# Kernel tuning notes

Hardware: AMD Instinct MI355X
Metric: run time of the kernel (lower is better)

The kernel has to match this reference:

```python
import jax, jax.numpy as jnp
import numpy as np

K = 3
P = 14
INV_SQRT2 = 0.7071067811865476  # db1 (Haar) filter coefficient
EPS = 1e-4


def _pool(x):
    # adaptive_avg_pool2d to (P, P); H, W divisible by P -> uniform mean pooling
    N, C, H, W = x.shape
    return x.reshape(N, C, P, H // P, P, W // P).mean(axis=(3, 5))


def setup_inputs() -> dict:
    key = jax.random.key(0)
    ks = jax.random.split(key, 8)
    N, C, H, W = 64, 3, 224, 224
    D, Cin = 540, 30  # D_clip=D_hidden=540, n_bands*3 = 30
    return {
        "frames": jax.random.normal(ks[0], (N, C, H, W), jnp.float32),
        "t_clip": jax.random.normal(ks[1], (N, D, P, P), jnp.float32),
        "w1": jax.random.normal(ks[2], (D, Cin), jnp.float32) * 0.05,
        "b1": jnp.zeros((D,), jnp.float32),
        "w2": jax.random.normal(ks[3], (D, D), jnp.float32) * 0.05,
        "b2": jnp.zeros((D,), jnp.float32),
        "wg": jax.random.normal(ks[4], (D, 2 * D, 3, 3), jnp.float32) * 0.05,
        "bg": jnp.zeros((D,), jnp.float32),
    }


def reference(frames, t_clip, w1, b1, w2, b2, wg, bg):
    # Batched Haar SWT2 (a trous, periodic), levels 1..K, fully vectorized over
    # (N, C) -- replaces the per-frame/per-channel pywt.swt2 CPU loop.
    a = frames
    bands = []  # per level: HL (cH), LH (cV), HH (cD), each (N, C, H, W)
    for j in range(K):
        d = 2 ** j  # filter dilation at level j+1
        lx = (a + jnp.roll(a, -d, axis=-1)) * INV_SQRT2
        hx = (a - jnp.roll(a, -d, axis=-1)) * INV_SQRT2
        cA = (lx + jnp.roll(lx, -d, axis=-2)) * INV_SQRT2
        cH = (lx - jnp.roll(lx, -d, axis=-2)) * INV_SQRT2
        cV = (hx + jnp.roll(hx, -d, axis=-2)) * INV_SQRT2
        cD = (hx - jnp.roll(hx, -d, axis=-2)) * INV_SQRT2
        bands += [cH, cV, cD]
        a = cA
    # per-(frame, channel) 99th-percentile normalization + pool to (P, P)
    pooled = []
    for b in bands:
        s = jnp.quantile(jnp.abs(b), 0.99, axis=(-2, -1), keepdims=True)
        pooled.append(_pool(b / (s + EPS)))
    # LL band (level K approximation): mean-center then quantile-scale
    mu = a.mean(axis=(-2, -1), keepdims=True)
    s = jnp.quantile(jnp.abs(a - mu), 0.99, axis=(-2, -1), keepdims=True)
    pooled.append(_pool((a - mu) / (s + EPS)))
    e_pix = jnp.concatenate(pooled, axis=1)  # (N, 30, P, P)

    # 1x1 conv -> relu -> 1x1 conv -> tanh
    h = jax.nn.relu(jnp.einsum("ncpq,dc->ndpq", e_pix, w1) + b1[None, :, None, None])
    m = jnp.tanh(jnp.einsum("ncpq,dc->ndpq", h, w2) + b2[None, :, None, None])

    # gated fusion with CLIP patch tokens
    gi = jnp.concatenate([t_clip, m], axis=1)  # (N, 2*D, P, P)
    g = jax.lax.conv_general_dilated(
        gi, wg, (1, 1), "SAME", dimension_numbers=("NCHW", "OIHW", "NCHW")
    ) + bg[None, :, None, None]
    gamma = jax.nn.sigmoid(g)
    return t_clip + gamma * m
```

## Files before the change

kernel.cpp:

```cpp
#include <hip/hip_runtime.h>

typedef unsigned short u16;
typedef unsigned int u32;
typedef __bf16 bf16x8 __attribute__((ext_vector_type(8)));
typedef float f32x4 __attribute__((ext_vector_type(4)));

constexpr int NB = 64, CH3 = 3;
constexpr int PLANES = NB * CH3;
constexpr int PPIX = 224 * 224;
constexpr int PP = 196;
constexpr int NPX = NB * PP;
constexpr int K2 = 576;
constexpr int CIPAD = 1088;
constexpr int KCONV = 9 * CIPAD;
constexpr int BINS = 256;
constexpr int BIN0 = 896;
constexpr int RANK1 = 49674;
constexpr int RANK2 = 49675;

constexpr size_t OFF_HIST = 0;
constexpr size_t SZ_HIST  = (size_t)10 * PLANES * BINS * 4;
constexpr size_t OFF_SUMS = OFF_HIST + SZ_HIST;
constexpr size_t OFF_INVS = OFF_SUMS + 768;
constexpr size_t OFF_BSUM = OFF_INVS + 7680;
constexpr size_t SZ_BSUM  = (size_t)10 * PLANES * PP * 4;
constexpr size_t OFF_EPIX = OFF_BSUM + SZ_BSUM;
constexpr size_t OFF_HBF  = OFF_EPIX + (size_t)NPX * 32 * 4;
constexpr size_t OFF_GIT  = OFF_HBF + (size_t)NPX * K2 * 2;
constexpr size_t SZ_GIT   = (size_t)NB * 256 * CIPAD * 2;
constexpr size_t OFF_WGB  = OFF_GIT + SZ_GIT;
constexpr size_t OFF_W2B  = OFF_WGB + (size_t)640 * KCONV * 2;
constexpr size_t OFF_MARR = OFF_W2B + (size_t)640 * K2 * 2;

__device__ __forceinline__ u16 f2bf(float x) {
  union { float f; u32 u; } c; c.f = x;
  u32 r = c.u + 0x7FFFu + ((c.u >> 16) & 1u);
  return (u16)(r >> 16);
}

__device__ __forceinline__ float wred64(float v) {
  v += __shfl_down(v, 32, 64); v += __shfl_down(v, 16, 64);
  v += __shfl_down(v, 8, 64);  v += __shfl_down(v, 4, 64);
  v += __shfl_down(v, 2, 64);  v += __shfl_down(v, 1, 64);
  return v;
}

__device__ __forceinline__ float gred16(float v) {
  v += __shfl_down(v, 8, 16); v += __shfl_down(v, 4, 16);
  v += __shfl_down(v, 2, 16); v += __shfl_down(v, 1, 16);
  return v;
}

__device__ __forceinline__ int hbin(float v) {
  int b = (int)(__float_as_uint(fabsf(v)) >> 20) - BIN0;
  return min(max(b, 0), BINS - 1);
}

__device__ __forceinline__ void cp16(const void* g, void* l) {
  __builtin_amdgcn_global_load_lds((const __attribute__((address_space(1))) u32*)g,
                                   (__attribute__((address_space(3))) u32*)l, 16, 0, 0);
}

#define BAR_MEM() asm volatile("s_barrier" ::: "memory")

constexpr int RSTRIDE = 10 * 128 + 8;
__global__ __launch_bounds__(256) void swt_fused_kernel(const float* __restrict__ frames,
    float* __restrict__ sums, int* __restrict__ hist, float* __restrict__ bsum)
{
  __shared__ float a1[22 * 224];
  __shared__ float a2[20 * 224];
  __shared__ u32 lh[8 * RSTRIDE];
  __shared__ float csum[14 * 10];
  __shared__ float wsum[4];
  const int t = threadIdx.x;
  const int rb = blockIdx.x, plane = blockIdx.y;
  const float* Pp = frames + (size_t)plane * PPIX;

  for (int i = t; i < 8 * RSTRIDE; i += 256) lh[i] = 0;
  __syncthreads();

  u32* lhr = &lh[(t & 7) * RSTRIDE];
  const int cell0 = (t >> 4) * 10;
  float ps = 0.f;

  if (t < 224) {
    int c2 = t + 1; if (c2 >= 224) c2 -= 224;
    float sH = 0.f, sV = 0.f, sD = 0.f;
    int gr0 = rb * 16; if (gr0 >= 224) gr0 -= 224;
    float q00 = Pp[gr0 * 224 + t], q01 = Pp[gr0 * 224 + c2];
    for (int r = 0; r < 22; ++r) {
      int gr1 = rb * 16 + r + 1; if (gr1 >= 224) gr1 -= 224;
      float p10 = Pp[gr1 * 224 + t], p11 = Pp[gr1 * 224 + c2];
      float sa = q00 + q01, sb = p10 + p11, da = q00 - q01, db = p10 - p11;
      a1[r * 224 + t] = (sa + sb) * 0.5f;
      if (r < 16) {
        float cH = (sa - sb) * 0.5f, cV = (da + db) * 0.5f, cD = (da - db) * 0.5f;
        int bH = hbin(cH), bV = hbin(cV), bD = hbin(cD);
        atomicAdd(&lhr[0 * 128 + (bH >> 1)], 1u << ((bH & 1) * 16));
        atomicAdd(&lhr[1 * 128 + (bV >> 1)], 1u << ((bV & 1) * 16));
        atomicAdd(&lhr[2 * 128 + (bD >> 1)], 1u << ((bD & 1) * 16));
        sH += cH; sV += cV; sD += cD;
        ps += q00;
      }
      q00 = p10; q01 = p11;
    }
    sH = gred16(sH); sV = gred16(sV); sD = gred16(sD);
    if ((t & 15) == 0) { csum[cell0 + 0] = sH; csum[cell0 + 1] = sV; csum[cell0 + 2] = sD; }
  }
  ps = wred64(ps);
  if ((t & 63) == 0) wsum[t >> 6] = ps;
  __syncthreads();
  if (t == 0) atomicAdd(&sums[plane], wsum[0] + wsum[1] + wsum[2] + wsum[3]);

  if (t < 224) {
    int c2 = t + 2; if (c2 >= 224) c2 -= 224;
    float sH = 0.f, sV = 0.f, sD = 0.f;
    for (int r = 0; r < 20; ++r) {
      float p00 = a1[r * 224 + t], p01 = a1[r * 224 + c2];
      float p10 = a1[(r + 2) * 224 + t], p11 = a1[(r + 2) * 224 + c2];
      float sa = p00 + p01, sb = p10 + p11, da = p00 - p01, db = p10 - p11;
      a2[r * 224 + t] = (sa + sb) * 0.5f;
      if (r < 16) {
        float cH = (sa - sb) * 0.5f, cV = (da + db) * 0.5f, cD = (da - db) * 0.5f;
        int bH = hbin(cH), bV = hbin(cV), bD = hbin(cD);
        atomicAdd(&lhr[3 * 128 + (bH >> 1)], 1u << ((bH & 1) * 16));
        atomicAdd(&lhr[4 * 128 + (bV >> 1)], 1u << ((bV & 1) * 16));
        atomicAdd(&lhr[5 * 128 + (bD >> 1)], 1u << ((bD & 1) * 16));
        sH += cH; sV += cV; sD += cD;
      }
    }
    sH = gred16(sH); sV = gred16(sV); sD = gred16(sD);
    if ((t & 15) == 0) { csum[cell0 + 3] = sH; csum[cell0 + 4] = sV; csum[cell0 + 5] = sD; }
  }
  __syncthreads();

  if (t < 224) {
    int c2 = t + 4; if (c2 >= 224) c2 -= 224;
    float sH = 0.f, sV = 0.f, sD = 0.f, sA = 0.f;
    for (int r = 0; r < 16; ++r) {
      float p00 = a2[r * 224 + t], p01 = a2[r * 224 + c2];
      float p10 = a2[(r + 4) * 224 + t], p11 = a2[(r + 4) * 224 + c2];
      float sa = p00 + p01, sb = p10 + p11, da = p00 - p01, db = p10 - p11;
      float cA = (sa + sb) * 0.5f;
      float cH = (sa - sb) * 0.5f, cV = (da + db) * 0.5f, cD = (da - db) * 0.5f;
      int bH = hbin(cH), bV = hbin(cV), bD = hbin(cD), bA = hbin(cA);
      atomicAdd(&lhr[6 * 128 + (bH >> 1)], 1u << ((bH & 1) * 16));
      atomicAdd(&lhr[7 * 128 + (bV >> 1)], 1u << ((bV & 1) * 16));
      atomicAdd(&lhr[8 * 128 + (bD >> 1)], 1u << ((bD & 1) * 16));
      atomicAdd(&lhr[9 * 128 + (bA >> 1)], 1u << ((bA & 1) * 16));
      sH += cH; sV += cV; sD += cD; sA += cA;
    }
    sH = gred16(sH); sV = gred16(sV); sD = gred16(sD); sA = gred16(sA);
    if ((t & 15) == 0) {
      csum[cell0 + 6] = sH; csum[cell0 + 7] = sV; csum[cell0 + 8] = sD; csum[cell0 + 9] = sA;
    }
  }
  __syncthreads();

  for (int i = t; i < 10 * 256; i += 256) {
    int bg = i >> 8, b = i & 255;
    u32 acc = 0;
#pragma unroll
    for (int rp = 0; rp < 8; ++rp)
      acc += (lh[rp * RSTRIDE + bg * 128 + (b >> 1)] >> ((b & 1) * 16)) & 0xFFFFu;
    if (acc) atomicAdd(&hist[((size_t)bg * PLANES + plane) * BINS + b], (int)acc);
  }
  if (t < 140) {
    int cell = t / 10, bg = t - cell * 10;
    bsum[((size_t)bg * PLANES + plane) * PP + rb * 14 + cell] = csum[cell * 10 + bg];
  }
}

__global__ __launch_bounds__(256) void quant_kernel(const int* __restrict__ hist,
    float* __restrict__ invs)
{
  const int g = blockIdx.x;
  __shared__ int cum[BINS];
  __shared__ float vv[2];
  const int t = threadIdx.x;
  const int c = hist[(size_t)g * BINS + t];
  cum[t] = c;
  __syncthreads();
  for (int off = 1; off < BINS; off <<= 1) {
    int y = (t >= off) ? cum[t - off] : 0;
    __syncthreads();
    cum[t] += y;
    __syncthreads();
  }
  int inc = cum[t], prev = inc - c;
#pragma unroll
  for (int k = 0; k < 2; ++k) {
    int rank = k ? RANK2 : RANK1;
    if (prev < rank && rank <= inc) {
      float lo = __uint_as_float((u32)(t + BIN0) << 20);
      float hi = __uint_as_float((u32)(t + BIN0 + 1) << 20);
      float fr = ((float)(rank - prev) - 0.5f) / (float)c;
      fr = fminf(fmaxf(fr, 0.f), 1.f);
      vv[k] = lo + (hi - lo) * fr;
    }
  }
  __syncthreads();
  if (t == 0) {
    float s = 0.75f * vv[0] + 0.25f * vv[1];
    invs[g] = 1.f / (s + 1e-4f);
  }
}

__global__ __launch_bounds__(256) void epix_kernel(const float* __restrict__ bsum,
    const float* __restrict__ sums, const float* __restrict__ invs, float* __restrict__ epix)
{
  int tid = blockIdx.x * 256 + threadIdx.x;
  int ch = tid & 31, px = tid >> 5;
  int n = px / PP, q = px - n * PP;
  float val = 0.f;
  if (ch < 27) {
    int bg = ch / 3, c = ch - bg * 3;
    int plane = n * 3 + c;
    val = bsum[((size_t)bg * PLANES + plane) * PP + q] * (1.f / 256.f) * invs[bg * PLANES + plane];
  } else if (ch < 30) {
    int c = ch - 27, plane = n * 3 + c;
    float mu = sums[plane] * (8.f / 50176.f);
    val = (bsum[((size_t)9 * PLANES + plane) * PP + q] * (1.f / 256.f) - mu) * invs[9 * PLANES + plane];
  }
  epix[tid] = val;
}

__global__ __launch_bounds__(256) void zero_halo_kernel(u16* __restrict__ git)
{
  constexpr int CPB = 136;
  constexpr int CPN = 60 * CPB + 196;
  int tid = blockIdx.x * 256 + threadIdx.x;
  if (tid >= NB * CPN) return;
  int n = tid / CPN, rem = tid - n * CPN;
  int y, x, c;
  if (rem < 60 * CPB) {
    int bi = rem / CPB; c = rem - bi * CPB;
    if (bi < 16) { y = 0; x = bi; }
    else if (bi < 32) { y = 15; x = bi - 16; }
    else { int i = bi - 32; y = 1 + (i >> 1); x = (i & 1) * 15; }
  } else {
    int q = rem - 60 * CPB;
    y = 1 + q / 14; x = 1 + q % 14; c = 135;
  }
  f32x4 z = (f32x4){0.f, 0.f, 0.f, 0.f};
  *reinterpret_cast<f32x4*>(&git[((size_t)(n * 256 + y * 16 + x)) * CIPAD + c * 8]) = z;
}

__global__ __launch_bounds__(256) void pack_wg_kernel(const float* __restrict__ wg,
    u16* __restrict__ wgb)
{
  __shared__ float w[9720];
  const int oc = blockIdx.x;
  const int t = threadIdx.x;
  if (oc < 540) {
    for (int i = t; i < 9720; i += 256) w[i] = wg[(size_t)oc * 9720 + i];
  }
  __syncthreads();
  for (int j = t; j < KCONV; j += 256) {
    int kc = j >> 6, i = j & 63;
    int cib = kc / 9, tap = kc - cib * 9;
    int ci = cib * 64 + i;
    float v = (oc < 540 && ci < 1080) ? w[ci * 9 + tap] : 0.f;
    wgb[(size_t)oc * KCONV + j] = f2bf(v);
  }
}

__global__ __launch_bounds__(256) void pack_w2_kernel(const float* __restrict__ w2,
    u16* __restrict__ w2b)
{
  int tid = blockIdx.x * 256 + threadIdx.x;
  int oc = tid / K2, cc = tid - oc * K2;
  float v = (oc < 540 && cc < 540) ? w2[oc * 540 + cc] : 0.f;
  w2b[tid] = f2bf(v);
}

__global__ __launch_bounds__(256) void fill_git_kernel(const float* __restrict__ tclip,
    u16* __restrict__ git)
{
  __shared__ float tile[64][65];
  const int n = blockIdx.z, ct = blockIdx.y, qt = blockIdx.x;
  const int t = threadIdx.x, tr = t >> 6, tc = t & 63;
#pragma unroll 4
  for (int i = 0; i < 16; ++i) {
    int ci = ct * 64 + i * 4 + tr, q = qt * 64 + tc;
    float v = (ci < 540 && q < 196) ? tclip[((size_t)n * 540 + ci) * 196 + q] : 0.f;
    tile[i * 4 + tr][tc] = v;
  }
  __syncthreads();
#pragma unroll 4
  for (int i = 0; i < 16; ++i) {
    int q = qt * 64 + i * 4 + tr, ci = ct * 64 + tc;
    if (q < 196 && ci < 540) {
      int y = q / 14, x = q - y * 14;
      git[(((size_t)n * 16 + 1 + y) * 16 + 1 + x) * CIPAD + ci] = f2bf(tile[tc][i * 4 + tr]);
    }
  }
}

__global__ __launch_bounds__(256) void gemm1_kernel(const float* __restrict__ epix,
    const float* __restrict__ w1, const float* __restrict__ b1, u16* __restrict__ hbf)
{
  __shared__ float es[64][33];
  __shared__ float w1s[128][33];
  const int t = threadIdx.x;
  const int px0 = blockIdx.x * 64, oc0 = blockIdx.y * 128;
  for (int i = t; i < 64 * 32; i += 256) { int r = i >> 5, cc = i & 31; es[r][cc] = epix[(size_t)(px0 + r) * 32 + cc]; }
  for (int i = t; i < 128 * 32; i += 256) {
    int r = i >> 5, cc = i & 31; int oc = oc0 + r;
    w1s[r][cc] = (oc < 540 && cc < 30) ? w1[oc * 30 + cc] : 0.f;
  }
  __syncthreads();
  const int ocl = t & 31, pxl = (t >> 5) * 8;
  float acc[4][8];
#pragma unroll
  for (int i = 0; i < 4; ++i)
#pragma unroll
    for (int j = 0; j < 8; ++j) acc[i][j] = 0.f;
  for (int k = 0; k < 30; ++k) {
    float wv[4], ev[8];
#pragma unroll
    for (int i = 0; i < 4; ++i) wv[i] = w1s[ocl + 32 * i][k];
#pragma unroll
    for (int j = 0; j < 8; ++j) ev[j] = es[pxl + j][k];
#pragma unroll
    for (int i = 0; i < 4; ++i)
#pragma unroll
      for (int j = 0; j < 8; ++j) acc[i][j] += wv[i] * ev[j];
  }
#pragma unroll
  for (int i = 0; i < 4; ++i) {
    int oc = oc0 + ocl + 32 * i;
    if (oc >= 576) continue;
    float bv = (oc < 540) ? b1[oc] : 0.f;
#pragma unroll
    for (int j = 0; j < 8; ++j) {
      int px = px0 + pxl + j;
      float v = (oc < 540) ? fmaxf(acc[i][j] + bv, 0.f) : 0.f;
      hbf[(size_t)px * K2 + oc] = f2bf(v);
    }
  }
}

template <int MODE>
__global__ __launch_bounds__(256) void mfma_gemm_kernel(
    const u16* __restrict__ A, const u16* __restrict__ Bm,
    const float* __restrict__ bias,
    float* __restrict__ marr, u16* __restrict__ git,
    const float* __restrict__ tclip, float* __restrict__ outp)
{
  constexpr int KCPB = (MODE == 1) ? 153 : 9;
  constexpr int BSTRIDE = (MODE == 1) ? KCONV : K2;
  __shared__ u16 smem[32768];
  const int t = threadIdx.x;
  const int lane = t & 63, wave = t >> 6;
  const int wm = wave & 1, wn = wave >> 1;

  int px0, oc0;
  if constexpr (MODE == 1) {
    int orig = blockIdx.x;
    int xcd = orig & 7, off = orig >> 3;
    constexpr int q = 61, r = 2;
    int wg = (xcd < r ? xcd * (q + 1) : r * (q + 1) + (xcd - r) * q) + off;
    int bx = wg / 5, by = wg - bx * 5;
    px0 = bx * 128; oc0 = by * 128;
  } else {
    px0 = blockIdx.x * 128; oc0 = blockIdx.y * 128;
  }

  const u16* aSrc[4];
  const u16* bSrc[4];
  int dstOff[4];
#pragma unroll
  for (int r = 0; r < 4; ++r) {
    int slot = r * 256 + t;
    int row = slot >> 3;
    int gs = ((slot ^ row) & 7) << 3;
    if constexpr (MODE == 0) {
      aSrc[r] = A + (size_t)(px0 + row) * K2 + gs;
    } else {
      int px = px0 + row;
      int n = px / 196, q2 = px - n * 196;
      int y = q2 / 14, x = q2 - y * 14;
      aSrc[r] = A + (size_t)((n * 16 + y) * 16 + x) * CIPAD + gs;
    }
    bSrc[r] = Bm + (size_t)(oc0 + row) * BSTRIDE + gs;
    dstOff[r] = (r * 256 + wave * 64) * 8;
  }

  auto stage = [&](int kcg, int buf) {
    int boff = kcg * 64;
    int aoff;
    if constexpr (MODE == 1) {
      int cib = kcg / 9, tap = kcg - cib * 9;
      int ky = tap / 3, kx = tap - ky * 3;
      aoff = (ky * 16 + kx) * CIPAD + cib * 64;
    } else aoff = boff;
    u16* As = smem + buf * 16384;
    u16* Bs = As + 8192;
#pragma unroll
    for (int r = 0; r < 4; ++r) cp16(aSrc[r] + aoff, As + dstOff[r]);
#pragma unroll
    for (int r = 0; r < 4; ++r) cp16(bSrc[r] + boff, Bs + dstOff[r]);
  };

  const int tx = lane & 15, quad = lane >> 4, l7 = lane & 7;
  int rowA[4], rowB[4];
#pragma unroll
  for (int i = 0; i < 4; ++i) {
    rowA[i] = (wm * 64 + i * 16 + tx) * 64;
    rowB[i] = (wn * 64 + i * 16 + tx) * 64;
  }

  f32x4 acc[4][4];
#pragma unroll
  for (int i = 0; i < 4; ++i)
#pragma unroll
    for (int j = 0; j < 4; ++j) acc[i][j] = (f32x4){0.f, 0.f, 0.f, 0.f};

  stage(0, 0);
  stage(1, 1);
  int cur = 0;
  for (int kc = 0; kc < KCPB; ++kc) {
    if (kc + 1 < KCPB) { asm volatile("s_waitcnt vmcnt(8)" ::: "memory"); }
    else               { asm volatile("s_waitcnt vmcnt(0)" ::: "memory"); }
    BAR_MEM();
    const u16* As = smem + cur * 16384;
    const u16* Bs = As + 8192;
#pragma unroll
    for (int ks = 0; ks < 2; ++ks) {
      int goff = (((ks * 4 + quad) ^ l7) << 3);
      bf16x8 af[4], bfr[4];
#pragma unroll
      for (int i = 0; i < 4; ++i) af[i] = *reinterpret_cast<const bf16x8*>(As + rowA[i] + goff);
#pragma unroll
      for (int i = 0; i < 4; ++i) bfr[i] = *reinterpret_cast<const bf16x8*>(Bs + rowB[i] + goff);
      __builtin_amdgcn_s_setprio(1);
#pragma unroll
      for (int i = 0; i < 4; ++i)
#pragma unroll
        for (int j = 0; j < 4; ++j)
          acc[i][j] = __builtin_amdgcn_mfma_f32_16x16x32_bf16(af[i], bfr[j], acc[i][j], 0, 0, 0);
      __builtin_amdgcn_s_setprio(0);
    }
    BAR_MEM();
    if (kc + 2 < KCPB) stage(kc + 2, cur);
    cur ^= 1;
  }

#pragma unroll
  for (int j = 0; j < 4; ++j) {
    int oc = oc0 + wn * 64 + j * 16 + tx;
    if (oc >= 540) continue;
    float bv = bias[oc];
#pragma unroll
    for (int i = 0; i < 4; ++i) {
      f32x4 v = acc[i][j];
      int px = px0 + wm * 64 + i * 16 + quad * 4;
      int n = px / 196, q2 = px - n * 196;
      size_t idx = ((size_t)(n * 540 + oc)) * 196 + q2;
      if constexpr (MODE == 0) {
#pragma unroll
        for (int r = 0; r < 4; ++r) {
          float val = tanhf(v[r] + bv);
          marr[idx + r] = val;
          int qq = q2 + r;
          int y = qq / 14, x = qq - y * 14;
          git[((n * 16 + 1 + y) * 16 + 1 + x) * CIPAD + 540 + oc] = f2bf(val);
        }
      } else {
        f32x4 mv = *reinterpret_cast<const f32x4*>(marr + idx);
        f32x4 tv = *reinterpret_cast<const f32x4*>(tclip + idx);
        f32x4 res;
#pragma unroll
        for (int r = 0; r < 4; ++r) {
          float g = v[r] + bv;
          res[r] = tv[r] + mv[r] / (1.f + expf(-g));
        }
        *reinterpret_cast<f32x4*>(outp + idx) = res;
      }
    }
  }
}

extern "C" void kernel_launch(void* const* d_in, const int* in_sizes, int n_in,
                              void* d_out, int out_size, void* d_ws, size_t ws_size,
                              hipStream_t stream)
{
  const float* frames = (const float*)d_in[0];
  const float* t_clip = (const float*)d_in[1];
  const float* w1 = (const float*)d_in[2];
  const float* b1 = (const float*)d_in[3];
  const float* w2 = (const float*)d_in[4];
  const float* b2 = (const float*)d_in[5];
  const float* wg = (const float*)d_in[6];
  const float* bg = (const float*)d_in[7];
  float* out = (float*)d_out;
  char* ws = (char*)d_ws;

  int* HIST = (int*)(ws + OFF_HIST);
  float* SUMS = (float*)(ws + OFF_SUMS);
  float* INVS = (float*)(ws + OFF_INVS);
  float* BSUM = (float*)(ws + OFF_BSUM);
  float* EPIX = (float*)(ws + OFF_EPIX);
  u16* HBF = (u16*)(ws + OFF_HBF);
  u16* GIT = (u16*)(ws + OFF_GIT);
  u16* WGB = (u16*)(ws + OFF_WGB);
  u16* W2B = (u16*)(ws + OFF_W2B);
  float* MARR = (float*)(ws + OFF_MARR);

  hipMemsetAsync(ws + OFF_HIST, 0, SZ_HIST + 768, stream);

  zero_halo_kernel<<<(NB * (60 * 136 + 196) + 255) / 256, 256, 0, stream>>>(GIT);
  pack_wg_kernel<<<640, 256, 0, stream>>>(wg, WGB);
  pack_w2_kernel<<<1440, 256, 0, stream>>>(w2, W2B);
  fill_git_kernel<<<dim3(4, 9, 64), 256, 0, stream>>>(t_clip, GIT);

  swt_fused_kernel<<<dim3(14, PLANES), 256, 0, stream>>>(frames, SUMS, HIST, BSUM);
  quant_kernel<<<1920, 256, 0, stream>>>(HIST, INVS);
  epix_kernel<<<1568, 256, 0, stream>>>(BSUM, SUMS, INVS, EPIX);

  gemm1_kernel<<<dim3(196, 5), 256, 0, stream>>>(EPIX, w1, b1, HBF);
  mfma_gemm_kernel<0><<<dim3(98, 5), 256, 0, stream>>>(HBF, W2B, b2, MARR, GIT, nullptr, nullptr);
  mfma_gemm_kernel<1><<<490, 256, 0, stream>>>(GIT, WGB, bg, MARR, nullptr, t_clip, out);
}
```

Measured before the change: 484.5 us.

## Load GEMM A fragments directly from global, merge pack kernels, fuse epix into gemm1

The MFMA GEMM kernels no longer stage the A operand (activations / im2col'd input) through LDS. Each lane reads its bf16x8 fragments straight from global memory, while B stays double-buffered in LDS, which halves shared memory and the async-copy count. The three weight-pack and halo-zero kernels become one launch, and the epix normalization is computed inside gemm1's tile load, which removes a kernel and an intermediate buffer. The risk is that uncached, uncoalesced per-lane global A loads in the big conv GEMM expose latency and cost bandwidth that LDS staging used to hide.

New measurement: 671.8 us. 38.6% more time.

```diff
diff --git a/kernel.cpp b/kernel.cpp
--- a/kernel.cpp
+++ b/kernel.cpp
@@ -206,72 +206,50 @@
   }
 }
 
-__global__ __launch_bounds__(256) void epix_kernel(const float* __restrict__ bsum,
-    const float* __restrict__ sums, const float* __restrict__ invs, float* __restrict__ epix)
-{
-  int tid = blockIdx.x * 256 + threadIdx.x;
-  int ch = tid & 31, px = tid >> 5;
-  int n = px / PP, q = px - n * PP;
-  float val = 0.f;
-  if (ch < 27) {
-    int bg = ch / 3, c = ch - bg * 3;
-    int plane = n * 3 + c;
-    val = bsum[((size_t)bg * PLANES + plane) * PP + q] * (1.f / 256.f) * invs[bg * PLANES + plane];
-  } else if (ch < 30) {
-    int c = ch - 27, plane = n * 3 + c;
-    float mu = sums[plane] * (8.f / 50176.f);
-    val = (bsum[((size_t)9 * PLANES + plane) * PP + q] * (1.f / 256.f) - mu) * invs[9 * PLANES + plane];
-  }
-  epix[tid] = val;
-}
-
-__global__ __launch_bounds__(256) void zero_halo_kernel(u16* __restrict__ git)
-{
-  constexpr int CPB = 136;
-  constexpr int CPN = 60 * CPB + 196;
-  int tid = blockIdx.x * 256 + threadIdx.x;
-  if (tid >= NB * CPN) return;
-  int n = tid / CPN, rem = tid - n * CPN;
-  int y, x, c;
-  if (rem < 60 * CPB) {
-    int bi = rem / CPB; c = rem - bi * CPB;
-    if (bi < 16) { y = 0; x = bi; }
-    else if (bi < 32) { y = 15; x = bi - 16; }
-    else { int i = bi - 32; y = 1 + (i >> 1); x = (i & 1) * 15; }
+__global__ __launch_bounds__(256) void pack_all_kernel(const float* __restrict__ wg,
+    const float* __restrict__ w2, u16* __restrict__ wgb, u16* __restrict__ w2b,
+    u16* __restrict__ git)
+{
+  __shared__ float w[9720];
+  const int bid = blockIdx.x;
+  const int t = threadIdx.x;
+  if (bid < 640) {
+    const int oc = bid;
+    if (oc < 540) {
+      for (int i = t; i < 9720; i += 256) w[i] = wg[(size_t)oc * 9720 + i];
+    }
+    __syncthreads();
+    for (int j = t; j < KCONV; j += 256) {
+      int kc = j >> 6, i = j & 63;
+      int cib = kc / 9, tap = kc - cib * 9;
+      int ci = cib * 64 + i;
+      float v = (oc < 540 && ci < 1080) ? w[ci * 9 + tap] : 0.f;
+      wgb[(size_t)oc * KCONV + j] = f2bf(v);
+    }
+  } else if (bid < 2080) {
+    int tid = (bid - 640) * 256 + t;
+    int oc = tid / K2, cc = tid - oc * K2;
+    float v = (oc < 540 && cc < 540) ? w2[oc * 540 + cc] : 0.f;
+    w2b[tid] = f2bf(v);
   } else {
-    int q = rem - 60 * CPB;
-    y = 1 + q / 14; x = 1 + q % 14; c = 135;
-  }
-  f32x4 z = (f32x4){0.f, 0.f, 0.f, 0.f};
-  *reinterpret_cast<f32x4*>(&git[((size_t)(n * 256 + y * 16 + x)) * CIPAD + c * 8]) = z;
-}
-
-__global__ __launch_bounds__(256) void pack_wg_kernel(const float* __restrict__ wg,
-    u16* __restrict__ wgb)
-{
-  __shared__ float w[9720];
-  const int oc = blockIdx.x;
-  const int t = threadIdx.x;
-  if (oc < 540) {
-    for (int i = t; i < 9720; i += 256) w[i] = wg[(size_t)oc * 9720 + i];
-  }
-  __syncthreads();
-  for (int j = t; j < KCONV; j += 256) {
-    int kc = j >> 6, i = j & 63;
-    int cib = kc / 9, tap = kc - cib * 9;
-    int ci = cib * 64 + i;
-    float v = (oc < 540 && ci < 1080) ? w[ci * 9 + tap] : 0.f;
-    wgb[(size_t)oc * KCONV + j] = f2bf(v);
-  }
-}
-
-__global__ __launch_bounds__(256) void pack_w2_kernel(const float* __restrict__ w2,
-    u16* __restrict__ w2b)
-{
-  int tid = blockIdx.x * 256 + threadIdx.x;
-  int oc = tid / K2, cc = tid - oc * K2;
-  float v = (oc < 540 && cc < 540) ? w2[oc * 540 + cc] : 0.f;
-  w2b[tid] = f2bf(v);
+    constexpr int CPB = 136;
+    constexpr int CPN = 60 * CPB + 196;
+    int tid = (bid - 2080) * 256 + t;
+    if (tid >= NB * CPN) return;
+    int n = tid / CPN, rem = tid - n * CPN;
+    int y, x, c;
+    if (rem < 60 * CPB) {
+      int bi = rem / CPB; c = rem - bi * CPB;
+      if (bi < 16) { y = 0; x = bi; }
+      else if (bi < 32) { y = 15; x = bi - 16; }
+      else { int i = bi - 32; y = 1 + (i >> 1); x = (i & 1) * 15; }
+    } else {
+      int q = rem - 60 * CPB;
+      y = 1 + q / 14; x = 1 + q % 14; c = 135;
+    }
+    f32x4 z = (f32x4){0.f, 0.f, 0.f, 0.f};
+    *reinterpret_cast<f32x4*>(&git[((size_t)(n * 256 + y * 16 + x)) * CIPAD + c * 8]) = z;
+  }
 }
 
 __global__ __launch_bounds__(256) void fill_git_kernel(const float* __restrict__ tclip,
@@ -297,14 +275,29 @@
   }
 }
 
-__global__ __launch_bounds__(256) void gemm1_kernel(const float* __restrict__ epix,
+__global__ __launch_bounds__(256) void gemm1_kernel(const float* __restrict__ bsum,
+    const float* __restrict__ sums, const float* __restrict__ invs,
     const float* __restrict__ w1, const float* __restrict__ b1, u16* __restrict__ hbf)
 {
   __shared__ float es[64][33];
   __shared__ float w1s[128][33];
   const int t = threadIdx.x;
   const int px0 = blockIdx.x * 64, oc0 = blockIdx.y * 128;
-  for (int i = t; i < 64 * 32; i += 256) { int r = i >> 5, cc = i & 31; es[r][cc] = epix[(size_t)(px0 + r) * 32 + cc]; }
+  for (int i = t; i < 64 * 32; i += 256) {
+    int r = i >> 5, cc = i & 31;
+    int px = px0 + r, n = px / PP, q = px - n * PP;
+    float val = 0.f;
+    if (cc < 27) {
+      int bg = cc / 3, c = cc - bg * 3;
+      int plane = n * 3 + c;
+      val = bsum[((size_t)bg * PLANES + plane) * PP + q] * (1.f / 256.f) * invs[bg * PLANES + plane];
+    } else if (cc < 30) {
+      int c = cc - 27, plane = n * 3 + c;
+      float mu = sums[plane] * (8.f / 50176.f);
+      val = (bsum[((size_t)9 * PLANES + plane) * PP + q] * (1.f / 256.f) - mu) * invs[9 * PLANES + plane];
+    }
+    es[r][cc] = val;
+  }
   for (int i = t; i < 128 * 32; i += 256) {
     int r = i >> 5, cc = i & 31; int oc = oc0 + r;
     w1s[r][cc] = (oc < 540 && cc < 30) ? w1[oc * 30 + cc] : 0.f;
@@ -350,7 +343,7 @@
 {
   constexpr int KCPB = (MODE == 1) ? 153 : 9;
   constexpr int BSTRIDE = (MODE == 1) ? KCONV : K2;
-  __shared__ u16 smem[32768];
+  __shared__ u16 smem[16384];
   const int t = threadIdx.x;
   const int lane = t & 63, wave = t >> 6;
   const int wm = wave & 1, wn = wave >> 1;
@@ -367,7 +360,8 @@
     px0 = blockIdx.x * 128; oc0 = blockIdx.y * 128;
   }
 
-  const u16* aSrc[4];
+  const int tx = lane & 15, quad = lane >> 4, l7 = lane & 7;
+
   const u16* bSrc[4];
   int dstOff[4];
 #pragma unroll
@@ -375,63 +369,62 @@
     int slot = r * 256 + t;
     int row = slot >> 3;
     int gs = ((slot ^ row) & 7) << 3;
+    bSrc[r] = Bm + (size_t)(oc0 + row) * BSTRIDE + gs;
+    dstOff[r] = (r * 256 + wave * 64) * 8;
+  }
+
+  const u16* Ag[4];
+#pragma unroll
+  for (int i = 0; i < 4; ++i) {
+    int px = px0 + wm * 64 + i * 16 + tx;
     if constexpr (MODE == 0) {
-      aSrc[r] = A + (size_t)(px0 + row) * K2 + gs;
+      Ag[i] = A + (size_t)px * K2;
     } else {
-      int px = px0 + row;
       int n = px / 196, q2 = px - n * 196;
       int y = q2 / 14, x = q2 - y * 14;
-      aSrc[r] = A + (size_t)((n * 16 + y) * 16 + x) * CIPAD + gs;
-    }
-    bSrc[r] = Bm + (size_t)(oc0 + row) * BSTRIDE + gs;
-    dstOff[r] = (r * 256 + wave * 64) * 8;
-  }
-
-  auto stage = [&](int kcg, int buf) {
+      Ag[i] = A + (size_t)((n * 16 + y) * 16 + x) * CIPAD;
+    }
+  }
+
+  auto stageB = [&](int kcg, int buf) {
     int boff = kcg * 64;
+    u16* Bs = smem + buf * 8192;
+#pragma unroll
+    for (int r = 0; r < 4; ++r) cp16(bSrc[r] + boff, Bs + dstOff[r]);
+  };
+
+  int rowB[4];
+#pragma unroll
+  for (int i = 0; i < 4; ++i) rowB[i] = (wn * 64 + i * 16 + tx) * 64;
+
+  f32x4 acc[4][4];
+#pragma unroll
+  for (int i = 0; i < 4; ++i)
+#pragma unroll
+    for (int j = 0; j < 4; ++j) acc[i][j] = (f32x4){0.f, 0.f, 0.f, 0.f};
+
+  stageB(0, 0);
+  stageB(1, 1);
+  int cur = 0;
+  for (int kc = 0; kc < KCPB; ++kc) {
+    if (kc + 1 < KCPB) { asm volatile("s_waitcnt vmcnt(4)" ::: "memory"); }
+    else               { asm volatile("s_waitcnt vmcnt(0)" ::: "memory"); }
+    BAR_MEM();
+    const u16* Bs = smem + cur * 8192;
     int aoff;
     if constexpr (MODE == 1) {
-      int cib = kcg / 9, tap = kcg - cib * 9;
+      int cib = kc / 9, tap = kc - cib * 9;
       int ky = tap / 3, kx = tap - ky * 3;
       aoff = (ky * 16 + kx) * CIPAD + cib * 64;
-    } else aoff = boff;
-    u16* As = smem + buf * 16384;
-    u16* Bs = As + 8192;
-#pragma unroll
-    for (int r = 0; r < 4; ++r) cp16(aSrc[r] + aoff, As + dstOff[r]);
-#pragma unroll
-    for (int r = 0; r < 4; ++r) cp16(bSrc[r] + boff, Bs + dstOff[r]);
-  };
-
-  const int tx = lane & 15, quad = lane >> 4, l7 = lane & 7;
-  int rowA[4], rowB[4];
-#pragma unroll
-  for (int i = 0; i < 4; ++i) {
-    rowA[i] = (wm * 64 + i * 16 + tx) * 64;
-    rowB[i] = (wn * 64 + i * 16 + tx) * 64;
-  }
-
-  f32x4 acc[4][4];
-#pragma unroll
-  for (int i = 0; i < 4; ++i)
-#pragma unroll
-    for (int j = 0; j < 4; ++j) acc[i][j] = (f32x4){0.f, 0.f, 0.f, 0.f};
-
-  stage(0, 0);
-  stage(1, 1);
-  int cur = 0;
-  for (int kc = 0; kc < KCPB; ++kc) {
-    if (kc + 1 < KCPB) { asm volatile("s_waitcnt vmcnt(8)" ::: "memory"); }
-    else               { asm volatile("s_waitcnt vmcnt(0)" ::: "memory"); }
-    BAR_MEM();
-    const u16* As = smem + cur * 16384;
-    const u16* Bs = As + 8192;
+    } else aoff = kc * 64;
 #pragma unroll
     for (int ks = 0; ks < 2; ++ks) {
+      int koff = (ks * 4 + quad) << 3;
       int goff = (((ks * 4 + quad) ^ l7) << 3);
       bf16x8 af[4], bfr[4];
 #pragma unroll
-      for (int i = 0; i < 4; ++i) af[i] = *reinterpret_cast<const bf16x8*>(As + rowA[i] + goff);
+      for (int i = 0; i < 4; ++i)
+        af[i] = *reinterpret_cast<const bf16x8*>(Ag[i] + aoff + koff);
 #pragma unroll
       for (int i = 0; i < 4; ++i) bfr[i] = *reinterpret_cast<const bf16x8*>(Bs + rowB[i] + goff);
       __builtin_amdgcn_s_setprio(1);
@@ -443,7 +436,7 @@
       __builtin_amdgcn_s_setprio(0);
     }
     BAR_MEM();
-    if (kc + 2 < KCPB) stage(kc + 2, cur);
+    if (kc + 2 < KCPB) stageB(kc + 2, cur);
     cur ^= 1;
   }
 
@@ -501,7 +494,6 @@
   float* SUMS = (float*)(ws + OFF_SUMS);
   float* INVS = (float*)(ws + OFF_INVS);
   float* BSUM = (float*)(ws + OFF_BSUM);
-  float* EPIX = (float*)(ws + OFF_EPIX);
   u16* HBF = (u16*)(ws + OFF_HBF);
   u16* GIT = (u16*)(ws + OFF_GIT);
   u16* WGB = (u16*)(ws + OFF_WGB);
@@ -510,16 +502,14 @@
 
   hipMemsetAsync(ws + OFF_HIST, 0, SZ_HIST + 768, stream);
 
-  zero_halo_kernel<<<(NB * (60 * 136 + 196) + 255) / 256, 256, 0, stream>>>(GIT);
-  pack_wg_kernel<<<640, 256, 0, stream>>>(wg, WGB);
-  pack_w2_kernel<<<1440, 256, 0, stream>>>(w2, W2B);
+  constexpr int HALO_BLOCKS = (NB * (60 * 136 + 196) + 255) / 256;
+  pack_all_kernel<<<2080 + HALO_BLOCKS, 256, 0, stream>>>(wg, w2, WGB, W2B, GIT);
   fill_git_kernel<<<dim3(4, 9, 64), 256, 0, stream>>>(t_clip, GIT);
 
   swt_fused_kernel<<<dim3(14, PLANES), 256, 0, stream>>>(frames, SUMS, HIST, BSUM);
   quant_kernel<<<1920, 256, 0, stream>>>(HIST, INVS);
-  epix_kernel<<<1568, 256, 0, stream>>>(BSUM, SUMS, INVS, EPIX);
-
-  gemm1_kernel<<<dim3(196, 5), 256, 0, stream>>>(EPIX, w1, b1, HBF);
+
+  gemm1_kernel<<<dim3(196, 5), 256, 0, stream>>>(BSUM, SUMS, INVS, w1, b1, HBF);
   mfma_gemm_kernel<0><<<dim3(98, 5), 256, 0, stream>>>(HBF, W2B, b2, MARR, GIT, nullptr, nullptr);
   mfma_gemm_kernel<1><<<490, 256, 0, stream>>>(GIT, WGB, bg, MARR, nullptr, t_clip, out);
 }
```
